# Optimization experiments

Hardware: AMD Instinct MI355X
Metric: run time of the kernel (lower is better)

Reference implementation:

```python
import jax, jax.numpy as jnp
import numpy as np

N = 131072          # events
N_OBS = 64          # observables
HID = [512, 512, 512]          # trunk hidden widths
SUB_HID = [512, 256]           # per-pair subnetwork hidden widths
P = 3                          # number of pairings


def _glorot(key, shape):
    fan_in, fan_out = shape[-2], shape[-1]
    lim = np.sqrt(6.0 / (fan_in + fan_out)).astype(np.float32)
    return jax.random.uniform(key, shape, jnp.float32, -lim, lim)


def setup_inputs() -> dict:
    key = jax.random.key(0)
    ks = jax.random.split(key, 16)
    x = jax.random.normal(ks[0], (N, N_OBS), jnp.float32)
    y = jax.random.randint(ks[1], (N,), 0, 3)
    pairs = jnp.array([[0, 1], [0, 2], [1, 2]], dtype=jnp.int32)
    # trunk params
    W0 = _glorot(ks[2], (N_OBS, HID[0])); b0 = jnp.zeros((HID[0],), jnp.float32)
    W1 = _glorot(ks[3], (HID[0], HID[1])); b1 = jnp.zeros((HID[1],), jnp.float32)
    W2 = _glorot(ks[4], (HID[1], HID[2])); b2 = jnp.zeros((HID[2],), jnp.float32)
    # stacked per-pair subnetwork params (all P subnets share shapes)
    SW0 = _glorot(ks[5], (P, HID[2], SUB_HID[0])); Sb0 = jnp.zeros((P, SUB_HID[0]), jnp.float32)
    SW1 = _glorot(ks[6], (P, SUB_HID[0], SUB_HID[1])); Sb1 = jnp.zeros((P, SUB_HID[1]), jnp.float32)
    SW2 = _glorot(ks[7], (P, SUB_HID[1], 1)); Sb2 = jnp.zeros((P, 1), jnp.float32)
    return {"x": x, "y": y, "pairs": pairs,
            "W0": W0, "b0": b0, "W1": W1, "b1": b1, "W2": W2, "b2": b2,
            "SW0": SW0, "Sb0": Sb0, "SW1": SW1, "Sb1": Sb1, "SW2": SW2, "Sb2": Sb2}


def reference(x, y, pairs, W0, b0, W1, b1, W2, b2, SW0, Sb0, SW1, Sb1, SW2, Sb2):
    relu = jax.nn.relu
    # Trunk. Note: in the torch module with dropout_prob>0, the first Linear sits at
    # layer index 1, so the activation is applied to the raw input as well (eval-mode
    # dropout == identity). We reproduce that exactly.
    h = relu(x) @ W0 + b0
    h = relu(h) @ W1 + b1
    repr_ = relu(h) @ W2 + b2                      # [N, HID[-1]]

    # Per-pair membership masks (jit-safe stand-in for the variable-size gather):
    # mask[p, n] = True iff y[n] is one of the two labels of pairing p.
    mask = (y[None, :] == pairs[:, 0:1]) | (y[None, :] == pairs[:, 1:2])  # [P, N] bool

    # Per-pair RatioModel subnetworks, batched over the pair dim.
    # Same activation-before-every-Linear pattern as the trunk (dropout indices).
    hs = jnp.einsum('nd,pdh->pnh', relu(repr_), SW0) + Sb0[:, None, :]
    hs = jnp.einsum('pnh,phk->pnk', relu(hs), SW1) + Sb1[:, None, :]
    logit = jnp.einsum('pnk,pko->pno', relu(hs), SW2) + Sb2[:, None, :]  # [P, N, 1]
    s_hat = jnp.clip(jax.nn.sigmoid(logit[..., 0]), 1e-9, None)          # [P, N]
    r_hat = (1.0 - s_hat) / s_hat                                        # [P, N]

    maskf = mask.astype(s_hat.dtype)
    return repr_, r_hat * maskf, s_hat * maskf, mask
```

## Files before the change

kernel.cpp:

```cpp
#include <hip/hip_runtime.h>
#include <stdint.h>

#define NE 131072

typedef __attribute__((ext_vector_type(8))) short bf16x8;
typedef __attribute__((ext_vector_type(4))) float f32x4;

static __device__ __forceinline__ unsigned short f2bf(float f) {
  unsigned u = __float_as_uint(f);
  u += 0x7FFF + ((u >> 16) & 1);
  return (unsigned short)(u >> 16);
}
static __device__ __forceinline__ float bf2f(unsigned short h) {
  return __uint_as_float((unsigned)h << 16);
}
static __device__ __forceinline__ void gload_lds16(const void* g, void* l) {
  __builtin_amdgcn_global_load_lds(
      (const __attribute__((address_space(1))) unsigned*)g,
      (__attribute__((address_space(3))) unsigned*)l, 16, 0, 0);
}

__global__ void weight_prep(const float* __restrict__ W0, const float* __restrict__ W1,
                            const float* __restrict__ W2, const float* __restrict__ SW0,
                            const float* __restrict__ SW1, const float* __restrict__ SW2,
                            unsigned short* W0t, unsigned short* W1t,
                            unsigned short* W2t, unsigned short* SW0t,
                            unsigned short* SW1t, unsigned short* SW2b) {
  __shared__ float tile[32][33];
  const int u = blockIdx.y;
  const float* src; unsigned short* dst; int K, Nc;
  if (u == 0)      { src = W0;  dst = W0t;  K = 64;  Nc = 512; }
  else if (u == 1) { src = W1;  dst = W1t;  K = 512; Nc = 512; }
  else if (u == 2) { src = W2;  dst = W2t;  K = 512; Nc = 512; }
  else if (u < 6)  { int p = u - 3; src = SW0 + (long)p * 512 * 512; dst = SW0t + (long)p * 512 * 512; K = 512; Nc = 512; }
  else if (u < 9)  { int p = u - 6; src = SW1 + (long)p * 512 * 256; dst = SW1t + (long)p * 256 * 512; K = 512; Nc = 256; }
  else             { int p = u - 9; src = SW2 + (long)p * 256;       dst = SW2b + (long)p * 256;       K = 256; Nc = 1; }
  const int tkn = K >> 5;
  const int tk = blockIdx.x % tkn, tn = blockIdx.x / tkn;
  if (tn >= ((Nc + 31) >> 5)) return;
  const int k0 = tk * 32, n0 = tn * 32;
  const int tx = threadIdx.x & 31, ty = threadIdx.x >> 5;
  if (n0 + tx < Nc)
#pragma unroll
    for (int j = 0; j < 4; ++j)
      tile[ty * 4 + j][tx] = src[(long)(k0 + ty * 4 + j) * Nc + n0 + tx];
  __syncthreads();
#pragma unroll
  for (int j = 0; j < 4; ++j) {
    int n = n0 + ty * 4 + j;
    if (n < Nc) dst[(long)n * K + k0 + tx] = f2bf(tile[tx][ty * 4 + j]);
  }
}

__global__ void relu_cvt_x(const float4* __restrict__ x,
                           ushort4* __restrict__ xb) {
  int i = blockIdx.x * blockDim.x + threadIdx.x;
  float4 v = x[i];
  ushort4 o;
  o.x = f2bf(fmaxf(v.x, 0.f));
  o.y = f2bf(fmaxf(v.y, 0.f));
  o.z = f2bf(fmaxf(v.z, 0.f));
  o.w = f2bf(fmaxf(v.w, 0.f));
  xb[i] = o;
}

__global__ void build_idx(const int* __restrict__ y, const int* __restrict__ pairs,
                          int chunkRows, int* __restrict__ idxL,
                          int* __restrict__ posA, int* __restrict__ cnts) {
  const int c = blockIdx.x, p = blockIdx.y;
  const int la = pairs[p * 2], lb = pairs[p * 2 + 1];
  const long r0 = (long)c * chunkRows;
  const long cb = r0;
  __shared__ int wbase[4];
  __shared__ int running;
  if (threadIdx.x == 0) running = 0;
  __syncthreads();
  const int lane = threadIdx.x & 63, wv = threadIdx.x >> 6;
  for (int it = 0; it < chunkRows / 256; ++it) {
    const int r = it * 256 + threadIdx.x;
    const int yv = y[r0 + r];
    const bool act = (yv == la) || (yv == lb);
    const unsigned long long m = __ballot(act);
    const int rank = __popcll(m & ((1ull << lane) - 1));
    if (lane == 0) wbase[wv] = __popcll(m);
    __syncthreads();
    int wb = 0;
#pragma unroll
    for (int w = 0; w < 4; ++w) wb += (w < wv) ? wbase[w] : 0;
    const int tot = wbase[0] + wbase[1] + wbase[2] + wbase[3];
    if (act) {
      const int posi = running + wb + rank;
      idxL[(long)p * NE + cb + posi] = r;
      posA[(long)p * NE + r0 + r] = (int)(cb + posi);
    } else {
      posA[(long)p * NE + r0 + r] = -1;
    }
    __syncthreads();
    if (threadIdx.x == 0) running += tot;
    __syncthreads();
  }
  const int cnt = running;
  if (threadIdx.x == 0) cnts[c * 3 + p] = cnt;
  const int padded = (cnt + 255) & ~255;
  const int last = (cnt > 0) ? idxL[(long)p * NE + cb + cnt - 1] : 0;
  for (int i = cnt + threadIdx.x; i < padded; i += 256)
    idxL[(long)p * NE + cb + i] = last;
}

__global__ __launch_bounds__(512, 4) void gemmT(
    const unsigned short* __restrict__ A, long aZ,
    const unsigned short* __restrict__ Bt, long bZ,
    const float* __restrict__ bias, long biasZ,
    float* __restrict__ outF,
    unsigned short* __restrict__ outA, long cZ,
    int K, int Nc,
    const unsigned short* __restrict__ w2, long w2Z,
    float* __restrict__ PB, long pbZ, int r0,
    const int* __restrict__ aIdx, long aIdxZ,
    const int* __restrict__ cnts) {
  __shared__ unsigned short lds[3 * 12288];
  __shared__ float part[4][128];
  const int z = blockIdx.z;
  const long brow = (long)blockIdx.x * 128;
  if (cnts) {
    const int cp = cnts[z];
    if ((int)brow >= ((cp + 255) & ~255)) return;
  }
  A += (long)z * aZ;
  Bt += (long)z * bZ;
  bias += (long)z * biasZ;
  if (outA) outA += (long)z * cZ;
  if (w2) { w2 += (long)z * w2Z; PB += (long)z * pbZ; }
  if (aIdx) aIdx += (long)z * aIdxZ;

  const int tid = threadIdx.x, wave = tid >> 6, lane = tid & 63;
  const int wm = wave >> 2, wn = wave & 3;
  const int lr = lane & 15, lh = lane >> 4;
  const int bcol = blockIdx.y * 256;
  const int nk = K >> 5;
  const int axr = (lh ^ ((lr >> 1) & 3)) * 8;

  const int arL = tid >> 2;
  const int arow = aIdx ? aIdx[brow + arL] : (int)(brow + arL);

  f32x4 acc[4][4];
#pragma unroll
  for (int m = 0; m < 4; ++m)
#pragma unroll
    for (int n = 0; n < 4; ++n) acc[m][n] = (f32x4){0.f, 0.f, 0.f, 0.f};

  auto STAGE = [&](int t) {
    if (t >= nk) return;
    unsigned short* dst = &lds[(t % 3) * 12288];
    const int k0 = t << 5;
    {
      const int c = tid;
      const int r = c >> 2;
      const int kc = (c & 3) ^ ((r >> 1) & 3);
      gload_lds16(A + (long)arow * K + k0 + kc * 8, &dst[(wave * 64) * 8]);
    }
#pragma unroll
    for (int i = 0; i < 2; ++i) {
      const int cb = i * 512 + wave * 64;
      const int c = cb + lane;
      const int r = c >> 2;
      const int kc = (c & 3) ^ ((r >> 1) & 3);
      gload_lds16(Bt + (long)(bcol + r) * K + k0 + kc * 8,
                  &dst[(512 + cb) * 8]);
    }
  };

  STAGE(0);
  STAGE(1);

  for (int t = 0; t < nk; ++t) {
    if (t < nk - 1)
      asm volatile("s_waitcnt vmcnt(3)" ::: "memory");
    else
      asm volatile("s_waitcnt vmcnt(0)" ::: "memory");
    __builtin_amdgcn_s_barrier();
    __builtin_amdgcn_sched_barrier(0);
    const unsigned short* buf = &lds[(t % 3) * 12288];
    bf16x8 a[4], b[4];
#pragma unroll
    for (int m = 0; m < 4; ++m)
      a[m] = *(const bf16x8*)&buf[(wm * 64 + m * 16 + lr) * 32 + axr];
#pragma unroll
    for (int n = 0; n < 4; ++n)
      b[n] = *(const bf16x8*)&buf[512 * 8 + (wn * 64 + n * 16 + lr) * 32 + axr];
    STAGE(t + 2);
    __builtin_amdgcn_s_setprio(1);
#pragma unroll
    for (int m = 0; m < 4; ++m)
#pragma unroll
      for (int n = 0; n < 4; ++n)
        acc[m][n] =
            __builtin_amdgcn_mfma_f32_16x16x32_bf16(a[m], b[n], acc[m][n], 0, 0, 0);
    __builtin_amdgcn_s_setprio(0);
  }

  float bv[4];
#pragma unroll
  for (int n = 0; n < 4; ++n) bv[n] = bias[bcol + wn * 64 + n * 16 + lr];

  if (!w2) {
#pragma unroll
    for (int m = 0; m < 4; ++m) {
#pragma unroll
      for (int r = 0; r < 4; ++r) {
        long e = brow + wm * 64 + m * 16 + lh * 4 + r;
#pragma unroll
        for (int n = 0; n < 4; ++n) {
          int oc = bcol + wn * 64 + n * 16 + lr;
          float v = acc[m][n][r] + bv[n];
          if (outF) outF[e * Nc + oc] = v;
          if (outA) outA[e * Nc + oc] = f2bf(fmaxf(v, 0.f));
        }
      }
    }
  } else {
    float w2v[4];
#pragma unroll
    for (int n = 0; n < 4; ++n) w2v[n] = bf2f(w2[wn * 64 + n * 16 + lr]);
#pragma unroll
    for (int m = 0; m < 4; ++m) {
#pragma unroll
      for (int r = 0; r < 4; ++r) {
        float s = 0.f;
#pragma unroll
        for (int n = 0; n < 4; ++n)
          s += fmaxf(acc[m][n][r] + bv[n], 0.f) * w2v[n];
#pragma unroll
        for (int off = 1; off < 16; off <<= 1) s += __shfl_xor(s, off);
        if (lr == 0) part[wn][wm * 64 + m * 16 + lh * 4 + r] = s;
      }
    }
    __syncthreads();
    if (tid < 128)
      PB[r0 + brow + tid] =
          part[0][tid] + part[1][tid] + part[2][tid] + part[3][tid];
  }
}

__global__ void head_final(const float* __restrict__ PB,
                           const int* __restrict__ posA,
                           const float* __restrict__ Sb2,
                           float* __restrict__ outR, float* __restrict__ outS,
                           float* __restrict__ outM) {
  const long n = (long)blockIdx.x * 256 + threadIdx.x;
  const int p = blockIdx.y;
  const int pos = posA[(long)p * NE + n];
  float rr = 0.f, s = 0.f, mf = 0.f;
  if (pos >= 0) {
    float logit = PB[(long)p * NE + pos] + Sb2[p];
    s = 1.f / (1.f + expf(-logit));
    s = fmaxf(s, 1e-9f);
    rr = (1.f - s) / s;
    mf = 1.f;
  }
  outR[(long)p * NE + n] = rr;
  outS[(long)p * NE + n] = s;
  outM[(long)p * NE + n] = mf;
}

extern "C" void kernel_launch(void* const* d_in, const int* in_sizes, int n_in,
                              void* d_out, int out_size, void* d_ws, size_t ws_size,
                              hipStream_t stream) {
  const float* x   = (const float*)d_in[0];
  const int*   y   = (const int*)d_in[1];
  const int*   prs = (const int*)d_in[2];
  const float* W0  = (const float*)d_in[3];
  const float* b0  = (const float*)d_in[4];
  const float* W1  = (const float*)d_in[5];
  const float* b1  = (const float*)d_in[6];
  const float* W2  = (const float*)d_in[7];
  const float* b2  = (const float*)d_in[8];
  const float* SW0 = (const float*)d_in[9];
  const float* Sb0 = (const float*)d_in[10];
  const float* SW1 = (const float*)d_in[11];
  const float* Sb1 = (const float*)d_in[12];
  const float* SW2 = (const float*)d_in[13];
  const float* Sb2 = (const float*)d_in[14];

  uint8_t* ws = (uint8_t*)d_ws;
  size_t off = 0;
  auto take = [&](size_t bytes) -> void* {
    void* ptr = ws + off;
    off = (off + bytes + 255) & ~(size_t)255;
    return ptr;
  };
  unsigned short* W0t  = (unsigned short*)take((size_t)64 * 512 * 2);
  unsigned short* W1t  = (unsigned short*)take((size_t)512 * 512 * 2);
  unsigned short* W2t  = (unsigned short*)take((size_t)512 * 512 * 2);
  unsigned short* SW0t = (unsigned short*)take((size_t)3 * 512 * 512 * 2);
  unsigned short* SW1t = (unsigned short*)take((size_t)3 * 256 * 512 * 2);
  unsigned short* SW2b = (unsigned short*)take((size_t)3 * 256 * 2);
  unsigned short* Xb   = (unsigned short*)take((size_t)NE * 64 * 2);
  float*          PB   = (float*)take((size_t)3 * NE * 4);
  int*            idxL = (int*)take((size_t)3 * NE * 4);
  int*            posA = (int*)take((size_t)3 * NE * 4);
  int*            cnts = (int*)take((size_t)64 * 4);
  const size_t fixed = off;

  long chunk = 65536;
  while (chunk > 8192 && fixed + (size_t)6 * chunk * 1024 + 4096 > ws_size)
    chunk >>= 1;
  const int nchunks = (int)(NE / chunk);

  unsigned short* T0   = (unsigned short*)take((size_t)chunk * 512 * 2);
  unsigned short* T1   = (unsigned short*)take((size_t)chunk * 512 * 2);
  unsigned short* bufR = (unsigned short*)take((size_t)chunk * 512 * 2);
  unsigned short* H3   = (unsigned short*)take((size_t)3 * chunk * 512 * 2);

  float* out   = (float*)d_out;
  float* outRe = out;
  float* outR  = out + (size_t)NE * 512;
  float* outS  = outR + (size_t)3 * NE;
  float* outM  = outS + (size_t)3 * NE;

  weight_prep<<<dim3(256, 12), 256, 0, stream>>>(W0, W1, W2, SW0, SW1, SW2,
                                                 W0t, W1t, W2t, SW0t, SW1t, SW2b);
  relu_cvt_x<<<dim3(NE * 64 / 4 / 256), 256, 0, stream>>>((const float4*)x,
                                                          (ushort4*)Xb);
  build_idx<<<dim3(nchunks, 3), 256, 0, stream>>>(y, prs, (int)chunk,
                                                  idxL, posA, cnts);

  for (int c = 0; c < nchunks; ++c) {
    const long r0 = (long)c * chunk;
    gemmT<<<dim3(chunk / 128, 2, 1), 512, 0, stream>>>(
        Xb + r0 * 64, 0, W0t, 0, b0, 0, nullptr, T0, 0, 64, 512,
        nullptr, 0, nullptr, 0, 0, nullptr, 0, nullptr);
    gemmT<<<dim3(chunk / 128, 2, 1), 512, 0, stream>>>(
        T0, 0, W1t, 0, b1, 0, nullptr, T1, 0, 512, 512,
        nullptr, 0, nullptr, 0, 0, nullptr, 0, nullptr);
    gemmT<<<dim3(chunk / 128, 2, 1), 512, 0, stream>>>(
        T1, 0, W2t, 0, b2, 0, outRe + r0 * 512, bufR, 0, 512, 512,
        nullptr, 0, nullptr, 0, 0, nullptr, 0, nullptr);
    gemmT<<<dim3(chunk / 128, 2, 3), 512, 0, stream>>>(
        bufR, 0, SW0t, (long)512 * 512, Sb0, 512, nullptr,
        H3, (long)chunk * 512, 512, 512,
        nullptr, 0, nullptr, 0, 0, idxL + r0, NE, cnts + c * 3);
    gemmT<<<dim3(chunk / 128, 1, 3), 512, 0, stream>>>(
        H3, (long)chunk * 512, SW1t, (long)256 * 512, Sb1, 256, nullptr,
        nullptr, 0, 512, 256,
        SW2b, 256, PB, (long)NE, (int)r0, nullptr, 0, cnts + c * 3);
  }
  head_final<<<dim3(NE / 256, 3), 256, 0, stream>>>(PB, posA, Sb2,
                                                    outR, outS, outM);
}
```

Baseline: 754.3 us.

## Merge prep kernels into one launch, fix chunk size, nontemporal fp32 stores

Combines weight transpose/convert, input relu+bf16 conversion and index building into a single prep_all launch, which removes two kernel launches and their serialization gaps. The chunk size is hardcoded to 32768 rows instead of being derived from the workspace size, which changes the number of GEMM launches per chunk loop and drops the workspace-size safety check. The fp32 representation output now uses nontemporal stores so the large streamed output does not pollute cache.

```diff
diff --git a/kernel.cpp b/kernel.cpp
--- a/kernel.cpp
+++ b/kernel.cpp
@@ -2,6 +2,7 @@
 #include <stdint.h>
 
 #define NE 131072
+#define SBCH 32768
 
 typedef __attribute__((ext_vector_type(8))) short bf16x8;
 typedef __attribute__((ext_vector_type(4))) float f32x4;
@@ -20,14 +21,73 @@
       (__attribute__((address_space(3))) unsigned*)l, 16, 0, 0);
 }
 
-__global__ void weight_prep(const float* __restrict__ W0, const float* __restrict__ W1,
-                            const float* __restrict__ W2, const float* __restrict__ SW0,
-                            const float* __restrict__ SW1, const float* __restrict__ SW2,
-                            unsigned short* W0t, unsigned short* W1t,
-                            unsigned short* W2t, unsigned short* SW0t,
-                            unsigned short* SW1t, unsigned short* SW2b) {
+__global__ void prep_all(const float* __restrict__ W0, const float* __restrict__ W1,
+                         const float* __restrict__ W2, const float* __restrict__ SW0,
+                         const float* __restrict__ SW1, const float* __restrict__ SW2,
+                         unsigned short* W0t, unsigned short* W1t,
+                         unsigned short* W2t, unsigned short* SW0t,
+                         unsigned short* SW1t, unsigned short* SW2b,
+                         const float4* __restrict__ x, ushort4* __restrict__ xb,
+                         const int* __restrict__ y, const int* __restrict__ pairs,
+                         int* __restrict__ idxL, int* __restrict__ posA,
+                         int* __restrict__ cnts) {
+  const int u = blockIdx.y;
+  if (u == 12) {
+    const int tot = NE * 64 / 4;
+    for (int i = blockIdx.x * 256 + threadIdx.x; i < tot; i += 256 * 256) {
+      float4 v = x[i];
+      ushort4 o;
+      o.x = f2bf(fmaxf(v.x, 0.f));
+      o.y = f2bf(fmaxf(v.y, 0.f));
+      o.z = f2bf(fmaxf(v.z, 0.f));
+      o.w = f2bf(fmaxf(v.w, 0.f));
+      xb[i] = o;
+    }
+    return;
+  }
+  if (u == 13) {
+    if (blockIdx.x >= 12) return;
+    const int c = blockIdx.x & 3, p = blockIdx.x >> 2;
+    const int la = pairs[p * 2], lb = pairs[p * 2 + 1];
+    const long r0 = (long)c * SBCH;
+    const long cb = r0;
+    __shared__ int wbase[4];
+    __shared__ int running;
+    if (threadIdx.x == 0) running = 0;
+    __syncthreads();
+    const int lane = threadIdx.x & 63, wv = threadIdx.x >> 6;
+    for (int it = 0; it < SBCH / 256; ++it) {
+      const int r = it * 256 + threadIdx.x;
+      const int yv = y[r0 + r];
+      const bool act = (yv == la) || (yv == lb);
+      const unsigned long long m = __ballot(act);
+      const int rank = __popcll(m & ((1ull << lane) - 1));
+      if (lane == 0) wbase[wv] = __popcll(m);
+      __syncthreads();
+      int wb = 0;
+#pragma unroll
+      for (int w = 0; w < 4; ++w) wb += (w < wv) ? wbase[w] : 0;
+      const int tot = wbase[0] + wbase[1] + wbase[2] + wbase[3];
+      if (act) {
+        const int posi = running + wb + rank;
+        idxL[(long)p * NE + cb + posi] = r;
+        posA[(long)p * NE + r0 + r] = (int)(cb + posi);
+      } else {
+        posA[(long)p * NE + r0 + r] = -1;
+      }
+      __syncthreads();
+      if (threadIdx.x == 0) running += tot;
+      __syncthreads();
+    }
+    const int cnt = running;
+    if (threadIdx.x == 0) cnts[c * 3 + p] = cnt;
+    const int padded = (cnt + 255) & ~255;
+    const int last = (cnt > 0) ? idxL[(long)p * NE + cb + cnt - 1] : 0;
+    for (int i = cnt + threadIdx.x; i < padded; i += 256)
+      idxL[(long)p * NE + cb + i] = last;
+    return;
+  }
   __shared__ float tile[32][33];
-  const int u = blockIdx.y;
   const float* src; unsigned short* dst; int K, Nc;
   if (u == 0)      { src = W0;  dst = W0t;  K = 64;  Nc = 512; }
   else if (u == 1) { src = W1;  dst = W1t;  K = 512; Nc = 512; }
@@ -50,61 +110,6 @@
     int n = n0 + ty * 4 + j;
     if (n < Nc) dst[(long)n * K + k0 + tx] = f2bf(tile[tx][ty * 4 + j]);
   }
-}
-
-__global__ void relu_cvt_x(const float4* __restrict__ x,
-                           ushort4* __restrict__ xb) {
-  int i = blockIdx.x * blockDim.x + threadIdx.x;
-  float4 v = x[i];
-  ushort4 o;
-  o.x = f2bf(fmaxf(v.x, 0.f));
-  o.y = f2bf(fmaxf(v.y, 0.f));
-  o.z = f2bf(fmaxf(v.z, 0.f));
-  o.w = f2bf(fmaxf(v.w, 0.f));
-  xb[i] = o;
-}
-
-__global__ void build_idx(const int* __restrict__ y, const int* __restrict__ pairs,
-                          int chunkRows, int* __restrict__ idxL,
-                          int* __restrict__ posA, int* __restrict__ cnts) {
-  const int c = blockIdx.x, p = blockIdx.y;
-  const int la = pairs[p * 2], lb = pairs[p * 2 + 1];
-  const long r0 = (long)c * chunkRows;
-  const long cb = r0;
-  __shared__ int wbase[4];
-  __shared__ int running;
-  if (threadIdx.x == 0) running = 0;
-  __syncthreads();
-  const int lane = threadIdx.x & 63, wv = threadIdx.x >> 6;
-  for (int it = 0; it < chunkRows / 256; ++it) {
-    const int r = it * 256 + threadIdx.x;
-    const int yv = y[r0 + r];
-    const bool act = (yv == la) || (yv == lb);
-    const unsigned long long m = __ballot(act);
-    const int rank = __popcll(m & ((1ull << lane) - 1));
-    if (lane == 0) wbase[wv] = __popcll(m);
-    __syncthreads();
-    int wb = 0;
-#pragma unroll
-    for (int w = 0; w < 4; ++w) wb += (w < wv) ? wbase[w] : 0;
-    const int tot = wbase[0] + wbase[1] + wbase[2] + wbase[3];
-    if (act) {
-      const int posi = running + wb + rank;
-      idxL[(long)p * NE + cb + posi] = r;
-      posA[(long)p * NE + r0 + r] = (int)(cb + posi);
-    } else {
-      posA[(long)p * NE + r0 + r] = -1;
-    }
-    __syncthreads();
-    if (threadIdx.x == 0) running += tot;
-    __syncthreads();
-  }
-  const int cnt = running;
-  if (threadIdx.x == 0) cnts[c * 3 + p] = cnt;
-  const int padded = (cnt + 255) & ~255;
-  const int last = (cnt > 0) ? idxL[(long)p * NE + cb + cnt - 1] : 0;
-  for (int i = cnt + threadIdx.x; i < padded; i += 256)
-    idxL[(long)p * NE + cb + i] = last;
 }
 
 __global__ __launch_bounds__(512, 4) void gemmT(
@@ -213,7 +218,7 @@
         for (int n = 0; n < 4; ++n) {
           int oc = bcol + wn * 64 + n * 16 + lr;
           float v = acc[m][n][r] + bv[n];
-          if (outF) outF[e * Nc + oc] = v;
+          if (outF) __builtin_nontemporal_store(v, &outF[e * Nc + oc]);
           if (outA) outA[e * Nc + oc] = f2bf(fmaxf(v, 0.f));
         }
       }
@@ -300,11 +305,8 @@
   int*            idxL = (int*)take((size_t)3 * NE * 4);
   int*            posA = (int*)take((size_t)3 * NE * 4);
   int*            cnts = (int*)take((size_t)64 * 4);
-  const size_t fixed = off;
-
-  long chunk = 65536;
-  while (chunk > 8192 && fixed + (size_t)6 * chunk * 1024 + 4096 > ws_size)
-    chunk >>= 1;
+
+  const long chunk = SBCH;
   const int nchunks = (int)(NE / chunk);
 
   unsigned short* T0   = (unsigned short*)take((size_t)chunk * 512 * 2);
@@ -318,12 +320,9 @@
   float* outS  = outR + (size_t)3 * NE;
   float* outM  = outS + (size_t)3 * NE;
 
-  weight_prep<<<dim3(256, 12), 256, 0, stream>>>(W0, W1, W2, SW0, SW1, SW2,
-                                                 W0t, W1t, W2t, SW0t, SW1t, SW2b);
-  relu_cvt_x<<<dim3(NE * 64 / 4 / 256), 256, 0, stream>>>((const float4*)x,
-                                                          (ushort4*)Xb);
-  build_idx<<<dim3(nchunks, 3), 256, 0, stream>>>(y, prs, (int)chunk,
-                                                  idxL, posA, cnts);
+  prep_all<<<dim3(256, 14), 256, 0, stream>>>(
+      W0, W1, W2, SW0, SW1, SW2, W0t, W1t, W2t, SW0t, SW1t, SW2b,
+      (const float4*)x, (ushort4*)Xb, y, prs, idxL, posA, cnts);
 
   for (int c = 0; c < nchunks; ++c) {
     const long r0 = (long)c * chunk;
```

Result: faster. 674.3 us (-10.6%).
